# Optimization experiments

Measured on AMD Instinct MI355X. Metric: run time of the kernel, lower is better.

Reference implementation:

```python
import jax, jax.numpy as jnp
import numpy as np

K = 7      # kernel_size
PAD = 3    # padding ('same' with stride 1)
G = 16     # groups


def _unfold(x):
    """torch nn.Unfold equivalent, stride=1, dilation=1.
    Returns [B, C, K*K, H, W] with kernel positions ordered (kh, kw),
    matching torch's (c, kh, kw) channel-major layout after reshape."""
    B, C, H, W = x.shape
    xp = jnp.pad(x, ((0, 0), (0, 0), (PAD, PAD), (PAD, PAD)))
    patches = jnp.stack(
        [xp[:, :, i:i + H, j:j + W] for i in range(K) for j in range(K)],
        axis=2,
    )
    return patches


def setup_inputs() -> dict:
    key = jax.random.key(0)
    k1, k2, k3 = jax.random.split(key, 3)
    B, C, H, W = 4, 256, 64, 64
    x = jax.random.normal(k1, (B, C, H, W), dtype=jnp.float32)
    # 1x1 conv producing kernel_prod*groups = 49*16 = 784 channels (with bias)
    w_kernel = jax.random.normal(k2, (G * K * K, C), dtype=jnp.float32) * 0.05
    b_kernel = jax.random.normal(k3, (G * K * K,), dtype=jnp.float32) * 0.05
    return {"x": x, "w_kernel": w_kernel, "b_kernel": b_kernel}


def reference(x, w_kernel, b_kernel):
    B, C, H, W = x.shape
    Cg = C // G
    # unfolded input: [B, G, C//G, K*K, H, W]
    patches = _unfold(x).reshape(B, G, Cg, K * K, H, W)
    # dynamic per-pixel kernel: AvgPool(k=1) is identity at stride 1,
    # then 1x1 conv with bias -> [B, G*K*K, H, W]
    kern = jnp.einsum('bchw,kc->bkhw', x, w_kernel) + b_kernel[None, :, None, None]
    kern = kern.reshape(B, G, 1, K * K, H, W)
    # multiply and sum-reduce over kernel positions, flatten groups
    out = (patches * kern).sum(axis=3).reshape(B, C, H, W)
    return out
```

## Files before the change

### kernel.cpp

```cpp
#include <hip/hip_runtime.h>


#define B_   4
#define C_   256
#define G_   16
#define KK_  49
#define KS_  7
#define PD_  3

#define XP8_BYTES (B_*32*4096*8*2)
#define WBF_OFF   XP8_BYTES

#define SKW   28
#define HC_   70
#define HPOS  (10*HC_)

typedef __attribute__((ext_vector_type(8))) short bf16x8;
typedef __attribute__((ext_vector_type(4))) float f32x4;
typedef unsigned short ushort_t;

__device__ inline unsigned f2bf(float f) {
    unsigned u = __float_as_uint(f);
    u += 0x7FFF + ((u >> 16) & 1);
    return u >> 16;
}

__global__ __launch_bounds__(256)
void cvt_xp8(const float* __restrict__ x, const float* __restrict__ wk,
             ushort_t* __restrict__ xp8, unsigned* __restrict__ wbf) {
    const int t = threadIdx.x;
    if (blockIdx.x == 64) {
        const int slice = blockIdx.z * 4 + blockIdx.y;
        const float2* wk2 = (const float2*)wk;
        const int base = slice * 6272;
        for (int k = t; k < 6272; k += 256) {
            float2 v = wk2[base + k];
            wbf[base + k] = f2bf(v.x) | (f2bf(v.y) << 16);
        }
        return;
    }
    __shared__ float tile[64][65];
    const int p0 = blockIdx.x * 64;
    const int c0 = blockIdx.y * 64;
    const int b  = blockIdx.z;
    const int px_r = t & 63;
    #pragma unroll
    for (int i = 0; i < 16; ++i) {
        int ch = (t >> 6) + i * 4;
        tile[ch][px_r] = x[((size_t)(b * C_ + c0 + ch) << 12) + p0 + px_r];
    }
    __syncthreads();
    const int px = t & 63;
    const int ob = t >> 6;
    #pragma unroll
    for (int jj = 0; jj < 2; ++jj) {
        const int j = ob + jj * 4;
        unsigned u[4];
        #pragma unroll
        for (int k2 = 0; k2 < 4; ++k2) {
            float a0 = tile[j * 8 + 2 * k2][px];
            float a1 = tile[j * 8 + 2 * k2 + 1][px];
            u[k2] = f2bf(a0) | (f2bf(a1) << 16);
        }
        ushort_t* dst = xp8 + (((size_t)((b << 5) + (c0 >> 3) + j) << 12) + p0 + px) * 8;
        *(uint4*)dst = make_uint4(u[0], u[1], u[2], u[3]);
    }
}

__device__ inline uint4 stage_ld(const ushort_t* __restrict__ xp8,
                                 int b, int oct, int gy0, int e) {
    const int row = e / HC_;
    const int col = e - row * HC_;
    const int sy = gy0 + row - PD_;
    const int sx = col - PD_;
    if (sy >= 0 && sy < 64 && sx >= 0 && sx < 64)
        return *(const uint4*)(xp8 + (((size_t)((b << 5) + oct) << 12) + sy * 64 + sx) * 8);
    return make_uint4(0u, 0u, 0u, 0u);
}

__global__ __launch_bounds__(512, 4)
void inv_fused(const ushort_t* __restrict__ xp8,
               const ushort_t* __restrict__ wbf,
               const float* __restrict__ bk,
               float* __restrict__ out) {
    __shared__ unsigned kern2[256 * SKW];
    __shared__ unsigned halo4[2 * HPOS * 4];

    const int bid  = blockIdx.x;
    const int g    = bid >> 6;
    const int b    = (bid >> 4) & 3;
    const int tile = bid & 15;
    const int gy0  = tile * 4;
    const int p0   = tile * 256;

    const int tid  = threadIdx.x;
    const int wv   = tid >> 6;
    const int ln15 = tid & 15;
    const int quad = (tid & 63) >> 4;

    f32x4 acc[8];
    #pragma unroll
    for (int i = 0; i < 8; ++i) acc[i] = (f32x4){0.f, 0.f, 0.f, 0.f};

    const ushort_t* ap[4];
    #pragma unroll
    for (int mt = 0; mt < 4; ++mt) {
        int r = mt * 16 + ln15; if (r > KK_ - 1) r = KK_ - 1;
        ap[mt] = wbf + (size_t)(g * KK_ + r) * C_ + quad * 8;
    }
    const ushort_t* bp = xp8 + (((size_t)((b << 5) + quad) << 12) + p0 + wv * 32 + ln15) * 8;

    bf16x8 af[2][4], bf[3][2];
    #pragma unroll
    for (int mt = 0; mt < 4; ++mt)
        af[0][mt] = *(const bf16x8*)(ap[mt]);
    #pragma unroll
    for (int kb = 0; kb < 2; ++kb) {
        #pragma unroll
        for (int nt = 0; nt < 2; ++nt)
            bf[kb][nt] = *(const bf16x8*)(bp + ((size_t)(kb * 32) << 12) + nt * 128);
    }

    #pragma unroll
    for (int k = 0; k < 8; ++k) {
        const int ca = k & 1;
        const int cb = k % 3;
        if (k < 7) {
            const int cc = (k + 1) * 32;
            #pragma unroll
            for (int mt = 0; mt < 4; ++mt)
                af[ca ^ 1][mt] = *(const bf16x8*)(ap[mt] + cc);
        }
        if (k < 6) {
            const int cc = (k + 2) * 32;
            #pragma unroll
            for (int nt = 0; nt < 2; ++nt)
                bf[(k + 2) % 3][nt] = *(const bf16x8*)(bp + ((size_t)cc << 12) + nt * 128);
        }
        #pragma unroll
        for (int mt = 0; mt < 4; ++mt) {
            #pragma unroll
            for (int nt = 0; nt < 2; ++nt) {
                acc[mt * 2 + nt] = __builtin_amdgcn_mfma_f32_16x16x32_bf16(
                    af[ca][mt], bf[cb][nt], acc[mt * 2 + nt], 0, 0, 0);
            }
        }
    }

    uint4 h0 = stage_ld(xp8, b, 2 * g, gy0, tid);
    const int e1 = tid + 512;
    uint4 h1 = (e1 < HPOS) ? stage_ld(xp8, b, 2 * g, gy0, e1)
                           : stage_ld(xp8, b, 2 * g + 1, gy0, e1 - HPOS);
    const int e2 = tid + 1024;
    uint4 h2 = (e2 < 2 * HPOS) ? stage_ld(xp8, b, 2 * g + 1, gy0, e2 - HPOS)
                               : make_uint4(0u, 0u, 0u, 0u);

    #pragma unroll
    for (int mt = 0; mt < 3; ++mt) {
        const int m0 = mt * 16 + quad * 4;
        const float b0 = bk[g * KK_ + m0],     b1 = bk[g * KK_ + m0 + 1];
        const float b2 = bk[g * KK_ + m0 + 2], b3 = bk[g * KK_ + m0 + 3];
        #pragma unroll
        for (int nt = 0; nt < 2; ++nt) {
            const int p = wv * 32 + nt * 16 + ln15;
            uint2 d;
            d.x = f2bf(acc[mt * 2 + nt][0] + b0) | (f2bf(acc[mt * 2 + nt][1] + b1) << 16);
            d.y = f2bf(acc[mt * 2 + nt][2] + b2) | (f2bf(acc[mt * 2 + nt][3] + b3) << 16);
            *(uint2*)&kern2[p * SKW + mt * 8 + quad * 2] = d;
        }
    }
    if (quad == 0) {
        const float b48 = bk[g * KK_ + 48];
        #pragma unroll
        for (int nt = 0; nt < 2; ++nt) {
            const int p = wv * 32 + nt * 16 + ln15;
            kern2[p * SKW + 24] = f2bf(acc[6 + nt][0] + b48);
        }
    }

    *(uint4*)&halo4[tid * 4] = h0;
    *(uint4*)&halo4[(tid + 512) * 4] = h1;
    if (tid < 2 * HPOS - 1024) *(uint4*)&halo4[(tid + 1024) * 4] = h2;

    __syncthreads();

    const int pix = tid & 255;
    float kv[KK_];
    {
        const uint4* kr = (const uint4*)&kern2[pix * SKW];
        unsigned kd[28];
        #pragma unroll
        for (int q = 0; q < 7; ++q) {
            uint4 h = kr[q];
            kd[4*q] = h.x; kd[4*q+1] = h.y; kd[4*q+2] = h.z; kd[4*q+3] = h.w;
        }
        #pragma unroll
        for (int k = 0; k < KK_; ++k) {
            unsigned d = kd[k >> 1];
            kv[k] = __uint_as_float((k & 1) ? (d & 0xffff0000u) : (d << 16));
        }
    }

    const int ho = tid >> 8;
    const int py = pix >> 6, px = pix & 63;

    float a[8];
    #pragma unroll
    for (int q = 0; q < 8; ++q) a[q] = 0.f;
    #pragma unroll
    for (int kh = 0; kh < KS_; ++kh) {
        const uint4* hr = (const uint4*)&halo4[(ho * HPOS + (py + kh) * HC_ + px) * 4];
        #pragma unroll
        for (int kw = 0; kw < KS_; ++kw) {
            uint4 hv = hr[kw];
            float kk = kv[kh * KS_ + kw];
            a[0] = fmaf(__uint_as_float(hv.x << 16), kk, a[0]);
            a[1] = fmaf(__uint_as_float(hv.x),       kk, a[1]);
            a[2] = fmaf(__uint_as_float(hv.y << 16), kk, a[2]);
            a[3] = fmaf(__uint_as_float(hv.y),       kk, a[3]);
            a[4] = fmaf(__uint_as_float(hv.z << 16), kk, a[4]);
            a[5] = fmaf(__uint_as_float(hv.z),       kk, a[5]);
            a[6] = fmaf(__uint_as_float(hv.w << 16), kk, a[6]);
            a[7] = fmaf(__uint_as_float(hv.w),       kk, a[7]);
        }
    }
    const size_t o = ((size_t)(b * C_ + g * 16 + ho * 8) << 12) + p0 + pix;
    #pragma unroll
    for (int q = 0; q < 8; ++q)
        out[o + ((size_t)q << 12)] = a[q];
}

extern "C" void kernel_launch(void* const* d_in, const int* in_sizes, int n_in,
                              void* d_out, int out_size, void* d_ws, size_t ws_size,
                              hipStream_t stream) {
    const float* x  = (const float*)d_in[0];
    const float* wk = (const float*)d_in[1];
    const float* bk = (const float*)d_in[2];
    float* o = (float*)d_out;

    ushort_t* xp8 = (ushort_t*)d_ws;
    unsigned* wbf = (unsigned*)((char*)d_ws + WBF_OFF);

    cvt_xp8<<<dim3(65, 4, B_), dim3(256), 0, stream>>>(x, wk, xp8, wbf);
    inv_fused<<<dim3(1024), dim3(512), 0, stream>>>(
        xp8, (const ushort_t*)wbf, bk, o);
}
```

Baseline: 111.1 us.

## Store pre-padded bf16 input and read halo directly from global memory

The conversion kernel now writes the channel-octet bf16 layout into a 70x70 zero-padded plane, with an extra block per (batch, octet group) that zeroes the border. The fused kernel drops the shared-memory halo staging and its bounds-checked loads, reading the 7x7 neighbourhood straight from global/L2 memory with no boundary checks. The GEMM loop's software-pipelined register prefetch is replaced by simple per-iteration loads, and occupancy is raised to 8 blocks by freeing LDS. In exchange, each neighbourhood element is reloaded from cache up to 49 times instead of once from LDS. Load latency is no longer overlapped explicitly.

```diff
diff --git a/kernel.cpp b/kernel.cpp
--- a/kernel.cpp
+++ b/kernel.cpp
@@ -8,12 +8,12 @@
 #define KS_  7
 #define PD_  3
 
-#define XP8_BYTES (B_*32*4096*8*2)
+#define PROW  70
+#define POCT  (PROW*PROW)
+#define XP8_BYTES (B_*32*POCT*16)
 #define WBF_OFF   XP8_BYTES
 
 #define SKW   28
-#define HC_   70
-#define HPOS  (10*HC_)
 
 typedef __attribute__((ext_vector_type(8))) short bf16x8;
 typedef __attribute__((ext_vector_type(4))) float f32x4;
@@ -39,6 +39,29 @@
         }
         return;
     }
+    if (blockIdx.x == 65) {
+        const int b  = blockIdx.z;
+        const int o0 = blockIdx.y * 8;
+        const uint4 z = make_uint4(0u, 0u, 0u, 0u);
+        #pragma unroll
+        for (int o = 0; o < 8; ++o) {
+            ushort_t* base = xp8 + (size_t)((b << 5) + o0 + o) * POCT * 8;
+            for (int e = t; e < 804; e += 256) {
+                int row, col;
+                if (e < 420) {
+                    row = e / 70; col = e - row * 70;
+                    if (row >= 3) row += 64;
+                } else {
+                    int f = e - 420;
+                    row = 3 + f / 6;
+                    int m = f - (f / 6) * 6;
+                    col = (m < 3) ? m : 64 + m;
+                }
+                *(uint4*)(base + (row * PROW + col) * 8) = z;
+            }
+        }
+        return;
+    }
     __shared__ float tile[64][65];
     const int p0 = blockIdx.x * 64;
     const int c0 = blockIdx.y * 64;
@@ -62,29 +85,18 @@
             float a1 = tile[j * 8 + 2 * k2 + 1][px];
             u[k2] = f2bf(a0) | (f2bf(a1) << 16);
         }
-        ushort_t* dst = xp8 + (((size_t)((b << 5) + (c0 >> 3) + j) << 12) + p0 + px) * 8;
+        ushort_t* dst = xp8 + ((size_t)((b << 5) + (c0 >> 3) + j) * POCT
+                               + (blockIdx.x + 3) * PROW + 3 + px) * 8;
         *(uint4*)dst = make_uint4(u[0], u[1], u[2], u[3]);
     }
 }
 
-__device__ inline uint4 stage_ld(const ushort_t* __restrict__ xp8,
-                                 int b, int oct, int gy0, int e) {
-    const int row = e / HC_;
-    const int col = e - row * HC_;
-    const int sy = gy0 + row - PD_;
-    const int sx = col - PD_;
-    if (sy >= 0 && sy < 64 && sx >= 0 && sx < 64)
-        return *(const uint4*)(xp8 + (((size_t)((b << 5) + oct) << 12) + sy * 64 + sx) * 8);
-    return make_uint4(0u, 0u, 0u, 0u);
-}
-
-__global__ __launch_bounds__(512, 4)
+__global__ __launch_bounds__(512, 8)
 void inv_fused(const ushort_t* __restrict__ xp8,
                const ushort_t* __restrict__ wbf,
                const float* __restrict__ bk,
                float* __restrict__ out) {
     __shared__ unsigned kern2[256 * SKW];
-    __shared__ unsigned halo4[2 * HPOS * 4];
 
     const int bid  = blockIdx.x;
     const int g    = bid >> 6;
@@ -102,58 +114,38 @@
     #pragma unroll
     for (int i = 0; i < 8; ++i) acc[i] = (f32x4){0.f, 0.f, 0.f, 0.f};
 
-    const ushort_t* ap[4];
-    #pragma unroll
-    for (int mt = 0; mt < 4; ++mt) {
-        int r = mt * 16 + ln15; if (r > KK_ - 1) r = KK_ - 1;
-        ap[mt] = wbf + (size_t)(g * KK_ + r) * C_ + quad * 8;
-    }
-    const ushort_t* bp = xp8 + (((size_t)((b << 5) + quad) << 12) + p0 + wv * 32 + ln15) * 8;
-
-    bf16x8 af[2][4], bf[3][2];
-    #pragma unroll
-    for (int mt = 0; mt < 4; ++mt)
-        af[0][mt] = *(const bf16x8*)(ap[mt]);
-    #pragma unroll
-    for (int kb = 0; kb < 2; ++kb) {
-        #pragma unroll
-        for (int nt = 0; nt < 2; ++nt)
-            bf[kb][nt] = *(const bf16x8*)(bp + ((size_t)(kb * 32) << 12) + nt * 128);
-    }
+    const char* bbase = (const char*)xp8 + (size_t)b * 32 * POCT * 16;
+    const char* abase = (const char*)wbf + (size_t)g * KK_ * 512;
+
+    int vb0, vb1;
+    {
+        int gi0 = p0 + wv * 32 + ln15;
+        int gi1 = gi0 + 16;
+        vb0 = (quad * POCT + ((gi0 >> 6) + 3) * PROW + 3 + (gi0 & 63)) * 16;
+        vb1 = (quad * POCT + ((gi1 >> 6) + 3) * PROW + 3 + (gi1 & 63)) * 16;
+    }
+    int va  = ln15 * 512 + quad * 16;
+    int va3 = 48 * 512 + quad * 16;
 
     #pragma unroll
     for (int k = 0; k < 8; ++k) {
-        const int ca = k & 1;
-        const int cb = k % 3;
-        if (k < 7) {
-            const int cc = (k + 1) * 32;
-            #pragma unroll
-            for (int mt = 0; mt < 4; ++mt)
-                af[ca ^ 1][mt] = *(const bf16x8*)(ap[mt] + cc);
-        }
-        if (k < 6) {
-            const int cc = (k + 2) * 32;
-            #pragma unroll
-            for (int nt = 0; nt < 2; ++nt)
-                bf[(k + 2) % 3][nt] = *(const bf16x8*)(bp + ((size_t)cc << 12) + nt * 128);
-        }
-        #pragma unroll
-        for (int mt = 0; mt < 4; ++mt) {
-            #pragma unroll
-            for (int nt = 0; nt < 2; ++nt) {
-                acc[mt * 2 + nt] = __builtin_amdgcn_mfma_f32_16x16x32_bf16(
-                    af[ca][mt], bf[cb][nt], acc[mt * 2 + nt], 0, 0, 0);
-            }
-        }
-    }
-
-    uint4 h0 = stage_ld(xp8, b, 2 * g, gy0, tid);
-    const int e1 = tid + 512;
-    uint4 h1 = (e1 < HPOS) ? stage_ld(xp8, b, 2 * g, gy0, e1)
-                           : stage_ld(xp8, b, 2 * g + 1, gy0, e1 - HPOS);
-    const int e2 = tid + 1024;
-    uint4 h2 = (e2 < 2 * HPOS) ? stage_ld(xp8, b, 2 * g + 1, gy0, e2 - HPOS)
-                               : make_uint4(0u, 0u, 0u, 0u);
+        bf16x8 af0 = *(const bf16x8*)(abase + va);
+        bf16x8 af1 = *(const bf16x8*)(abase + 8192 + va);
+        bf16x8 af2 = *(const bf16x8*)(abase + 16384 + va);
+        bf16x8 af3 = *(const bf16x8*)(abase + va3);
+        bf16x8 bf0 = *(const bf16x8*)(bbase + vb0);
+        bf16x8 bf1 = *(const bf16x8*)(bbase + vb1);
+        acc[0] = __builtin_amdgcn_mfma_f32_16x16x32_bf16(af0, bf0, acc[0], 0, 0, 0);
+        acc[1] = __builtin_amdgcn_mfma_f32_16x16x32_bf16(af0, bf1, acc[1], 0, 0, 0);
+        acc[2] = __builtin_amdgcn_mfma_f32_16x16x32_bf16(af1, bf0, acc[2], 0, 0, 0);
+        acc[3] = __builtin_amdgcn_mfma_f32_16x16x32_bf16(af1, bf1, acc[3], 0, 0, 0);
+        acc[4] = __builtin_amdgcn_mfma_f32_16x16x32_bf16(af2, bf0, acc[4], 0, 0, 0);
+        acc[5] = __builtin_amdgcn_mfma_f32_16x16x32_bf16(af2, bf1, acc[5], 0, 0, 0);
+        acc[6] = __builtin_amdgcn_mfma_f32_16x16x32_bf16(af3, bf0, acc[6], 0, 0, 0);
+        acc[7] = __builtin_amdgcn_mfma_f32_16x16x32_bf16(af3, bf1, acc[7], 0, 0, 0);
+        va  += 64;  va3 += 64;
+        vb0 += 4 * POCT * 16; vb1 += 4 * POCT * 16;
+    }
 
     #pragma unroll
     for (int mt = 0; mt < 3; ++mt) {
@@ -178,42 +170,34 @@
         }
     }
 
-    *(uint4*)&halo4[tid * 4] = h0;
-    *(uint4*)&halo4[(tid + 512) * 4] = h1;
-    if (tid < 2 * HPOS - 1024) *(uint4*)&halo4[(tid + 1024) * 4] = h2;
-
     __syncthreads();
 
     const int pix = tid & 255;
-    float kv[KK_];
+    const int ho  = tid >> 8;
+    unsigned kd[28];
     {
         const uint4* kr = (const uint4*)&kern2[pix * SKW];
-        unsigned kd[28];
         #pragma unroll
         for (int q = 0; q < 7; ++q) {
             uint4 h = kr[q];
             kd[4*q] = h.x; kd[4*q+1] = h.y; kd[4*q+2] = h.z; kd[4*q+3] = h.w;
         }
-        #pragma unroll
-        for (int k = 0; k < KK_; ++k) {
-            unsigned d = kd[k >> 1];
-            kv[k] = __uint_as_float((k & 1) ? (d & 0xffff0000u) : (d << 16));
-        }
-    }
-
-    const int ho = tid >> 8;
+    }
+
     const int py = pix >> 6, px = pix & 63;
+    int vh = ((2 * g + ho) * POCT + (gy0 + py) * PROW + px) * 16;
 
     float a[8];
     #pragma unroll
     for (int q = 0; q < 8; ++q) a[q] = 0.f;
     #pragma unroll
     for (int kh = 0; kh < KS_; ++kh) {
-        const uint4* hr = (const uint4*)&halo4[(ho * HPOS + (py + kh) * HC_ + px) * 4];
         #pragma unroll
         for (int kw = 0; kw < KS_; ++kw) {
-            uint4 hv = hr[kw];
-            float kk = kv[kh * KS_ + kw];
+            uint4 hv = *(const uint4*)(bbase + vh + kw * 16);
+            const int t49 = kh * KS_ + kw;
+            unsigned d = kd[t49 >> 1];
+            float kk = __uint_as_float((t49 & 1) ? (d & 0xffff0000u) : (d << 16));
             a[0] = fmaf(__uint_as_float(hv.x << 16), kk, a[0]);
             a[1] = fmaf(__uint_as_float(hv.x),       kk, a[1]);
             a[2] = fmaf(__uint_as_float(hv.y << 16), kk, a[2]);
@@ -223,6 +207,7 @@
             a[6] = fmaf(__uint_as_float(hv.w << 16), kk, a[6]);
             a[7] = fmaf(__uint_as_float(hv.w),       kk, a[7]);
         }
+        vh += PROW * 16;
     }
     const size_t o = ((size_t)(b * C_ + g * 16 + ho * 8) << 12) + p0 + pix;
     #pragma unroll
@@ -241,7 +226,7 @@
     ushort_t* xp8 = (ushort_t*)d_ws;
     unsigned* wbf = (unsigned*)((char*)d_ws + WBF_OFF);
 
-    cvt_xp8<<<dim3(65, 4, B_), dim3(256), 0, stream>>>(x, wk, xp8, wbf);
+    cvt_xp8<<<dim3(66, 4, B_), dim3(256), 0, stream>>>(x, wk, xp8, wbf);
     inv_fused<<<dim3(1024), dim3(512), 0, stream>>>(
         xp8, (const ushort_t*)wbf, bk, o);
 }
```

New measurement: 117.7 us. 5.9% more time.
